# Performance work log

Hardware: AMD Instinct MI355X
Metric: run time of the kernel (lower is better)

Reference implementation:

```python
import jax, jax.numpy as jnp
import numpy as np
import math

D_MODEL = 1024
D_STATE = 16
D_CONV = 4
EXPAND = 2
D_INNER = EXPAND * D_MODEL
DT_RANK = 64
BATCH = 4
SEQ_LEN = 2048


def setup_inputs() -> dict:
    key = jax.random.key(0)
    ks = jax.random.split(key, 10)
    hidden_states = jax.random.normal(ks[0], (BATCH, SEQ_LEN, D_MODEL), jnp.float32)
    in_proj_w = jax.random.normal(ks[1], (D_MODEL, 2 * D_INNER), jnp.float32) * (D_MODEL ** -0.5)
    conv_w = jax.random.normal(ks[2], (D_INNER, D_CONV), jnp.float32) * (D_CONV ** -0.5)
    conv_b = jnp.zeros((D_INNER,), jnp.float32)
    x_proj_w = jax.random.normal(ks[3], (D_INNER, DT_RANK + 2 * D_STATE), jnp.float32) * (D_INNER ** -0.5)
    dt_init_std = DT_RANK ** -0.5
    dt_proj_w = jax.random.uniform(ks[4], (DT_RANK, D_INNER), jnp.float32, -dt_init_std, dt_init_std)
    # inverse-softplus init of dt bias: dt ~ logUniform(dt_min, dt_max)
    dt_min, dt_max, dt_floor = 0.001, 0.1, 1e-4
    dt = jnp.exp(jax.random.uniform(ks[5], (D_INNER,), jnp.float32) * (math.log(dt_max) - math.log(dt_min)) + math.log(dt_min))
    dt = jnp.clip(dt, dt_floor, None)
    dt_proj_b = dt + jnp.log(-jnp.expm1(-dt))
    A = jnp.tile(jnp.arange(1, D_STATE + 1, dtype=jnp.float32)[None, :], (D_INNER, 1))
    A_log = jnp.log(A)
    D = jnp.ones((D_INNER,), jnp.float32)
    out_proj_w = jax.random.normal(ks[6], (D_INNER, D_MODEL), jnp.float32) * (D_INNER ** -0.5)
    return {
        "hidden_states": hidden_states,
        "in_proj_w": in_proj_w,
        "conv_w": conv_w,
        "conv_b": conv_b,
        "x_proj_w": x_proj_w,
        "dt_proj_w": dt_proj_w,
        "dt_proj_b": dt_proj_b,
        "A_log": A_log,
        "D": D,
        "out_proj_w": out_proj_w,
    }


def _mamba_forward(hidden_states, in_proj_w, conv_w, conv_b, x_proj_w, dt_proj_w, dt_proj_b, A_log, D, out_proj_w):
    b, L, _ = hidden_states.shape
    d_state = A_log.shape[1]
    dt_rank = dt_proj_w.shape[0]
    K = conv_w.shape[1]

    xz = hidden_states @ in_proj_w                     # (b, L, 2*d_inner)
    x, z = jnp.split(xz, 2, axis=-1)                   # each (b, L, d_inner)

    # causal depthwise conv1d (padding = K-1, truncated to L)
    x_pad = jnp.pad(x, ((0, 0), (K - 1, 0), (0, 0)))
    x = sum(x_pad[:, k:k + L, :] * conv_w[:, k] for k in range(K)) + conv_b
    x = jax.nn.silu(x)

    x_dbl = x @ x_proj_w                               # (b, L, dt_rank + 2*d_state)
    dt, B, C = jnp.split(x_dbl, [dt_rank, dt_rank + d_state], axis=-1)
    dt = jax.nn.softplus(dt @ dt_proj_w + dt_proj_b)   # (b, L, d_inner)
    A = -jnp.exp(A_log)                                # (d_inner, d_state)

    def step(h, inp):
        x_t, dt_t, B_t, C_t = inp                      # (b,d), (b,d), (b,n), (b,n)
        dA = jnp.exp(A[None] * dt_t[..., None])        # (b, d, n)
        h = dA * h + dt_t[..., None] * B_t[:, None, :] * x_t[..., None]
        y_t = jnp.einsum('bdn,bn->bd', h, C_t) + D * x_t
        return h, y_t

    h0 = jnp.zeros((b, x.shape[-1], d_state), x.dtype)
    xs = (x.transpose(1, 0, 2), dt.transpose(1, 0, 2), B.transpose(1, 0, 2), C.transpose(1, 0, 2))
    _, ys = jax.lax.scan(step, h0, xs)                 # ys: (L, b, d_inner)
    y = ys.transpose(1, 0, 2) * jax.nn.silu(z)
    return y @ out_proj_w                              # (b, L, d_model)


def reference(hidden_states, in_proj_w, conv_w, conv_b, x_proj_w, dt_proj_w, dt_proj_b, A_log, D, out_proj_w):
    return _mamba_forward(hidden_states, in_proj_w, conv_w, conv_b, x_proj_w, dt_proj_w, dt_proj_b, A_log, D, out_proj_w)
```

## Files before the change

### kernel.cpp

```cpp
#include <hip/hip_runtime.h>
#include <hip/hip_bf16.h>


#define DM 1024
#define DS 16
#define DC 4
#define DI 2048
#define DR 64
#define NB 4
#define SL 2048
#define NTOK (NB*SL)
#define XDBL_W (DR + 2*DS)
#define CONV_R 8

typedef __hip_bfloat16 bf16;
typedef unsigned short u16;
typedef __attribute__((ext_vector_type(8))) short s8v;
typedef __attribute__((ext_vector_type(4))) float f4v;
typedef __attribute__((ext_vector_type(4))) unsigned short us4;

__device__ __forceinline__ float b2f(bf16 v) { return __bfloat162float(v); }
__device__ __forceinline__ bf16  f2b(float v) { return __float2bfloat16(v); }
__device__ __forceinline__ u16 f2u(float x) {
    union { bf16 h; u16 s; } u; u.h = f2b(x); return u.s;
}
__device__ __forceinline__ float u2f(u16 s) {
    union { bf16 h; u16 s; } u; u.s = s; return b2f(u.h);
}

__device__ __forceinline__ bool sniff_bf16(const void* Dones) {
    return ((const u16*)Dones)[0] == 0x3F80u;
}

__device__ __forceinline__ float softplus_fast(float v) {
    return fmaxf(v, 0.f) + __logf(1.f + __expf(-fabsf(v)));
}

template<int MODE>
__device__ __forceinline__ float ld(const void* p, size_t i, bool bf) {
    if (MODE == 0) return b2f(((const bf16*)p)[i]);
    if (MODE == 1) return ((const float*)p)[i];
    return bf ? b2f(((const bf16*)p)[i]) : ((const float*)p)[i];
}
template<int MODE>
__device__ __forceinline__ void st(void* p, size_t i, bool bf, float v) {
    if (MODE == 0)      { ((bf16*)p)[i] = f2b(v); }
    else if (MODE == 1) { ((float*)p)[i] = v; }
    else { if (bf) ((bf16*)p)[i] = f2b(v); else ((float*)p)[i] = v; }
}

template<int CM>
__device__ __forceinline__ void cstore(void* C, void* C2, size_t m, int n,
                                       int ldc, bool bf, float v) {
    if (CM == 3) {
        if (n < DR) ((bf16*)C2)[m * DR + n] = f2b(v);
        else        ((float*)C)[m * (2 * DS) + (n - DR)] = v;
    } else {
        st<CM>(C, m * (size_t)ldc + n, bf, v);
    }
}

#define AS1 __attribute__((address_space(1)))
#define AS3 __attribute__((address_space(3)))
__device__ __forceinline__ void gload_lds16(const void* g, void* l) {
    __builtin_amdgcn_global_load_lds((const AS1 unsigned int*)g,
                                     (AS3 unsigned int*)l, 16, 0, 0);
}

__global__ __launch_bounds__(256) void cast_bf16_kernel(
    const void* __restrict__ src, bf16* __restrict__ dst,
    const void* __restrict__ sniff)
{
    const bool bf = sniff_bf16(sniff);
    const size_t i = ((size_t)blockIdx.x * 256 + threadIdx.x) * 4;
    if (bf) {
        *(us4*)((u16*)dst + i) = *(const us4*)((const u16*)src + i);
    } else {
        const f4v f = *(const f4v*)((const float*)src + i);
        us4 o; o.x = f2u(f.x); o.y = f2u(f.y); o.z = f2u(f.z); o.w = f2u(f.w);
        *(us4*)((u16*)dst + i) = o;
    }
}

__global__ __launch_bounds__(256) void transpose_w(
    const void* __restrict__ w, bf16* __restrict__ wt,
    int K, int N, const void* __restrict__ sniff)
{
    const bool bf = sniff_bf16(sniff);
    __shared__ float t[32][33];
    const int tx = threadIdx.x & 31, ty = threadIdx.x >> 5;
    const int n0 = blockIdx.x * 32, k0 = blockIdx.y * 32;
    #pragma unroll
    for (int i = 0; i < 4; i++) {
        int k = k0 + ty + i * 8, n = n0 + tx;
        t[ty + i * 8][tx] = (n < N) ? ld<2>(w, (size_t)k * N + n, bf) : 0.f;
    }
    __syncthreads();
    #pragma unroll
    for (int i = 0; i < 4; i++) {
        int n = n0 + ty + i * 8, k = k0 + tx;
        wt[(size_t)n * K + k] = f2b(t[tx][ty + i * 8]);
    }
}

template<int CM, int EPI>
__global__ __launch_bounds__(256) void gemm_mfma(
    const bf16* __restrict__ A, int lda,
    const bf16* __restrict__ Bt,
    void* __restrict__ C, void* __restrict__ C2, int ldc,
    int M, int N, int K,
    const void* __restrict__ bias,
    const void* __restrict__ sniff)
{
    const bool bf = sniff_bf16(sniff);
    __shared__ short As[128 * 32];
    __shared__ short Bs[128 * 32];

    const int tid  = threadIdx.x;
    const int lane = tid & 63;
    const int wave = tid >> 6;
    const int wm = (wave & 1) * 64;
    const int wn = (wave >> 1) * 64;
    const int m0 = blockIdx.x * 128;
    const int n0 = blockIdx.y * 128;
    const int ll = lane & 15;
    const int qd = lane >> 4;

    const int srow  = lane >> 2;
    const int skoff = (lane & 3) * 8;

    const short* Ag = (const short*)A;
    const short* Bg = (const short*)Bt;
    char* AsB = (char*)As + wave * 2048 + lane * 16;
    char* BsB = (char*)Bs + wave * 2048 + lane * 16;
    const size_t a_row = (size_t)(m0 + wave * 32 + srow);
    const size_t b_row = (size_t)(n0 + wave * 32 + srow);

    f4v acc[4][4];
    #pragma unroll
    for (int i = 0; i < 4; i++)
        #pragma unroll
        for (int j = 0; j < 4; j++)
            acc[i][j] = (f4v){0.f, 0.f, 0.f, 0.f};

    for (int k0 = 0; k0 < K; k0 += 32) {
        gload_lds16(Ag + a_row * lda + k0 + skoff,            AsB);
        gload_lds16(Ag + (a_row + 16) * lda + k0 + skoff,     AsB + 1024);
        gload_lds16(Bg + b_row * K + k0 + skoff,              BsB);
        gload_lds16(Bg + (b_row + 16) * K + k0 + skoff,       BsB + 1024);
        __syncthreads();

        s8v af[4], bfr[4];
        #pragma unroll
        for (int s = 0; s < 4; s++)
            af[s] = *(const s8v*)&As[(wm + s * 16 + ll) * 32 + qd * 8];
        #pragma unroll
        for (int s = 0; s < 4; s++)
            bfr[s] = *(const s8v*)&Bs[(wn + s * 16 + ll) * 32 + qd * 8];
        #pragma unroll
        for (int i = 0; i < 4; i++)
            #pragma unroll
            for (int j = 0; j < 4; j++)
                acc[i][j] = __builtin_amdgcn_mfma_f32_16x16x32_bf16(
                    af[i], bfr[j], acc[i][j], 0, 0, 0);
        __syncthreads();
    }

    #pragma unroll
    for (int sn = 0; sn < 4; sn++) {
        const int cn = n0 + wn + sn * 16 + ll;
        if (cn >= N) continue;
        float bv = 0.f;
        if (EPI == 1) bv = ld<2>(bias, cn, bf);
        #pragma unroll
        for (int sm = 0; sm < 4; sm++) {
            #pragma unroll
            for (int r = 0; r < 4; r++) {
                const int cm = m0 + wm + sm * 16 + qd * 4 + r;
                float v = acc[sm][sn][r];
                if (EPI == 1) v = softplus_fast(v + bv);
                cstore<CM>(C, C2, (size_t)cm, cn, ldc, bf, v);
            }
        }
    }
}

template<int AM, int CM, int EPI>
__global__ __launch_bounds__(256) void gemm_kernel(
    const void* __restrict__ A, int lda,
    const void* __restrict__ B, size_t bbase, int ldb,
    void* __restrict__ C, void* __restrict__ C2, int ldc,
    int M, int N, int K,
    const void* __restrict__ bias,
    const void* __restrict__ sniff)
{
    const bool bf = sniff_bf16(sniff);
    const int BM = 64, BN = 64, BK = 16;
    __shared__ float Asm[BK][BM + 4];
    __shared__ float Bsm[BK][BN + 4];

    const int tid = threadIdx.x;
    const int m0 = blockIdx.x * BM;
    const int n0 = blockIdx.y * BN;
    const int tx = tid % 16;
    const int ty = tid / 16;
    const int a_k = tid % BK;
    const int a_m = tid / BK;
    const int b_n = tid % BN;
    const int b_k = tid / BN;

    float acc[4][4] = {};

    for (int k0 = 0; k0 < K; k0 += BK) {
        #pragma unroll
        for (int i = 0; i < 4; i++) {
            int m = m0 + a_m + i * 16;
            float v = 0.f;
            if (m < M) v = ld<AM>(A, (size_t)m * lda + (k0 + a_k), bf);
            Asm[a_k][a_m + i * 16] = v;
        }
        #pragma unroll
        for (int i = 0; i < 4; i++) {
            int kk = b_k + i * 4;
            int n = n0 + b_n;
            float v = 0.f;
            if (n < N) v = ld<2>(B, bbase + (size_t)(k0 + kk) * ldb + n, bf);
            Bsm[kk][b_n] = v;
        }
        __syncthreads();
        #pragma unroll
        for (int kk = 0; kk < BK; kk++) {
            float av[4], bv[4];
            #pragma unroll
            for (int i = 0; i < 4; i++) av[i] = Asm[kk][ty * 4 + i];
            #pragma unroll
            for (int j = 0; j < 4; j++) bv[j] = Bsm[kk][tx * 4 + j];
            #pragma unroll
            for (int i = 0; i < 4; i++)
                #pragma unroll
                for (int j = 0; j < 4; j++)
                    acc[i][j] += av[i] * bv[j];
        }
        __syncthreads();
    }
    #pragma unroll
    for (int i = 0; i < 4; i++) {
        int m = m0 + ty * 4 + i;
        if (m >= M) continue;
        #pragma unroll
        for (int j = 0; j < 4; j++) {
            int n = n0 + tx * 4 + j;
            if (n >= N) continue;
            float v = acc[i][j];
            if (EPI == 1) {
                v += ld<2>(bias, n, bf);
                v = softplus_fast(v);
            }
            cstore<CM>(C, C2, (size_t)m, n, ldc, bf, v);
        }
    }
}

__global__ __launch_bounds__(256) void conv_silu_kernel(
    const bf16* __restrict__ xg, const void* __restrict__ w,
    const void* __restrict__ bias, bf16* __restrict__ xc,
    const void* __restrict__ sniff)
{
    const bool bf = sniff_bf16(sniff);
    const int c  = blockIdx.x * 256 + threadIdx.x;
    const int r0 = blockIdx.y * CONV_R;
    const int l0 = r0 % SL;

    float w0, w1, w2, w3;
    if (bf) {
        const us4 wv = *(const us4*)((const u16*)w + (size_t)c * 4);
        w0 = u2f(wv.x); w1 = u2f(wv.y); w2 = u2f(wv.z); w3 = u2f(wv.w);
    } else {
        const f4v wv = *(const f4v*)((const float*)w + (size_t)c * 4);
        w0 = wv.x; w1 = wv.y; w2 = wv.z; w3 = wv.w;
    }
    const float bs = ld<2>(bias, c, bf);

    float xm3 = (l0 >= 3) ? b2f(xg[(size_t)(r0 - 3) * DI + c]) : 0.f;
    float xm2 = (l0 >= 2) ? b2f(xg[(size_t)(r0 - 2) * DI + c]) : 0.f;
    float xm1 = (l0 >= 1) ? b2f(xg[(size_t)(r0 - 1) * DI + c]) : 0.f;

    #pragma unroll
    for (int i = 0; i < CONV_R; i++) {
        const size_t row = (size_t)(r0 + i);
        const float x0 = b2f(xg[row * DI + c]);
        const float acc = bs + w0 * xm3 + w1 * xm2 + w2 * xm1 + w3 * x0;
        const float s = acc / (1.f + __expf(-acc));
        xc[row * DI + c] = f2b(s);
        xm3 = xm2; xm2 = xm1; xm1 = x0;
    }
}

__global__ __launch_bounds__(256) void scan_pass1(
    const bf16* __restrict__ xc, const bf16* __restrict__ dt,
    const float* __restrict__ bc,
    const void* __restrict__ A_log, const void* __restrict__ Dones,
    float* __restrict__ P, float* __restrict__ Q, int nch)
{
    const bool bf = sniff_bf16(Dones);
    const int d = blockIdx.x * 256 + threadIdx.x;
    const int c = blockIdx.y;
    const int b = blockIdx.z;
    const int T = SL / nch;

    float a[DS], Pp[DS], Qq[DS];
    bool lad = true;
    #pragma unroll
    for (int n = 0; n < DS; n++) {
        a[n] = -__expf(ld<2>(A_log, (size_t)d * DS + n, bf));
        Pp[n] = 1.f; Qq[n] = 0.f;
        lad = lad && (fabsf(a[n] - (n + 1) * a[0]) < 1e-3f);
    }

    const size_t base = (size_t)b * SL + (size_t)c * T;
    if (lad) {
        const float a0 = a[0];
        for (int i = 0; i < T; i++) {
            const size_t row = base + i;
            const float xv  = b2f(xc[row * DI + d]);
            const float dtv = b2f(dt[row * DI + d]);
            const float dtx = dtv * xv;
            const float* Bv = bc + row * (2 * DS);
            const float r = __expf(a0 * dtv);
            float cur = r;
            #pragma unroll
            for (int n = 0; n < DS; n++) {
                Pp[n] *= cur;
                Qq[n] = cur * Qq[n] + dtx * Bv[n];
                cur *= r;
            }
        }
    } else {
        for (int i = 0; i < T; i++) {
            const size_t row = base + i;
            const float xv  = b2f(xc[row * DI + d]);
            const float dtv = b2f(dt[row * DI + d]);
            const float dtx = dtv * xv;
            const float* Bv = bc + row * (2 * DS);
            #pragma unroll
            for (int n = 0; n < DS; n++) {
                const float dA = __expf(a[n] * dtv);
                Pp[n] *= dA;
                Qq[n] = dA * Qq[n] + dtx * Bv[n];
            }
        }
    }
    const size_t o = (((size_t)b * nch + c) * DI + d) * DS;
    #pragma unroll
    for (int n = 0; n < DS; n++) { P[o + n] = Pp[n]; Q[o + n] = Qq[n]; }
}

__global__ __launch_bounds__(256) void scan_pass2(
    float* __restrict__ P, const float* __restrict__ Q, int nch)
{
    const int j = blockIdx.x * 256 + threadIdx.x;
    const int b = blockIdx.y;
    float h = 0.f;
    for (int c = 0; c < nch; c++) {
        const size_t o = ((size_t)b * nch + c) * (DI * DS) + j;
        const float p = P[o];
        const float q = Q[o];
        P[o] = h;
        h = p * h + q;
    }
}

__global__ __launch_bounds__(256) void scan_pass3(
    const bf16* __restrict__ xc, const bf16* __restrict__ dt,
    const float* __restrict__ bc, bf16* __restrict__ z,
    const void* __restrict__ A_log, const void* __restrict__ Dones,
    const float* __restrict__ H, int nch)
{
    const bool bf = sniff_bf16(Dones);
    const int d = blockIdx.x * 256 + threadIdx.x;
    const int c = blockIdx.y;
    const int b = blockIdx.z;
    const int T = SL / nch;

    float a[DS], h[DS];
    bool lad = true;
    const size_t o = (((size_t)b * nch + c) * DI + d) * DS;
    #pragma unroll
    for (int n = 0; n < DS; n++) {
        a[n] = -__expf(ld<2>(A_log, (size_t)d * DS + n, bf));
        h[n] = H[o + n];
        lad = lad && (fabsf(a[n] - (n + 1) * a[0]) < 1e-3f);
    }
    const float dD = ld<2>(Dones, d, bf);
    const size_t base = (size_t)b * SL + (size_t)c * T;

    if (lad) {
        const float a0 = a[0];
        for (int i = 0; i < T; i++) {
            const size_t row = base + i;
            const float xv  = b2f(xc[row * DI + d]);
            const float dtv = b2f(dt[row * DI + d]);
            const float zv  = b2f(z[row * DI + d]);
            const float dtx = dtv * xv;
            const float* Bv = bc + row * (2 * DS);
            const float* Cv = Bv + DS;
            const float r = __expf(a0 * dtv);
            float cur = r;
            float y = dD * xv;
            #pragma unroll
            for (int n = 0; n < DS; n++) {
                h[n] = cur * h[n] + dtx * Bv[n];
                y += h[n] * Cv[n];
                cur *= r;
            }
            const float g = zv / (1.f + __expf(-zv));
            z[row * DI + d] = f2b(y * g);
        }
    } else {
        for (int i = 0; i < T; i++) {
            const size_t row = base + i;
            const float xv  = b2f(xc[row * DI + d]);
            const float dtv = b2f(dt[row * DI + d]);
            const float zv  = b2f(z[row * DI + d]);
            const float dtx = dtv * xv;
            const float* Bv = bc + row * (2 * DS);
            const float* Cv = Bv + DS;
            float y = dD * xv;
            #pragma unroll
            for (int n = 0; n < DS; n++) {
                const float dA = __expf(a[n] * dtv);
                h[n] = dA * h[n] + dtx * Bv[n];
                y += h[n] * Cv[n];
            }
            const float g = zv / (1.f + __expf(-zv));
            z[row * DI + d] = f2b(y * g);
        }
    }
}

__global__ __launch_bounds__(256) void scan_serial(
    const bf16* __restrict__ xc, const bf16* __restrict__ dt,
    const float* __restrict__ bc, bf16* __restrict__ z,
    const void* __restrict__ A_log, const void* __restrict__ Dones)
{
    const bool bf = sniff_bf16(Dones);
    const int d = blockIdx.x * 256 + threadIdx.x;
    const int b = blockIdx.y;
    float a[DS], h[DS];
    #pragma unroll
    for (int n = 0; n < DS; n++) {
        a[n] = -__expf(ld<2>(A_log, (size_t)d * DS + n, bf));
        h[n] = 0.f;
    }
    const float dD = ld<2>(Dones, d, bf);
    const size_t base = (size_t)b * SL;
    for (int l = 0; l < SL; l++) {
        const size_t row = base + l;
        const float xv  = b2f(xc[row * DI + d]);
        const float dtv = b2f(dt[row * DI + d]);
        const float* Bv = bc + row * (2 * DS);
        const float dtx = dtv * xv;
        float y = dD * xv;
        #pragma unroll
        for (int n = 0; n < DS; n++) {
            const float dA = __expf(a[n] * dtv);
            h[n] = dA * h[n] + dtx * Bv[n];
            y += h[n] * Bv[DS + n];
        }
        const float zv = b2f(z[row * DI + d]);
        const float g = zv / (1.f + __expf(-zv));
        z[row * DI + d] = f2b(y * g);
    }
}

extern "C" void kernel_launch(void* const* d_in, const int* in_sizes, int n_in,
                              void* d_out, int out_size, void* d_ws, size_t ws_size,
                              hipStream_t stream) {
    const void* hs        = d_in[0];
    const void* in_proj_w = d_in[1];
    const void* conv_w    = d_in[2];
    const void* conv_b    = d_in[3];
    const void* x_proj_w  = d_in[4];
    const void* dt_proj_w = d_in[5];
    const void* dt_proj_b = d_in[6];
    const void* A_log     = d_in[7];
    const void* Dones     = d_in[8];
    const void* out_proj_w= d_in[9];

    char* ws = (char*)d_ws;
    bf16*  xg   = (bf16*)(ws);
    bf16*  xc   = (bf16*)(ws + 33554432);
    bf16*  hsb  = (bf16*)(ws + 33554432);
    bf16*  z    = (bf16*)(ws + 67108864);
    float* bc   = (float*)(ws + 100663296);
    bf16*  dtf  = (bf16*)(ws + 101711872);
    const size_t WT_OFF = 102760448;
    bf16* in_projT  = (bf16*)(ws + WT_OFF);
    bf16* x_projT   = (bf16*)(ws + WT_OFF);
    bf16* dt_projT  = (bf16*)(ws + WT_OFF + 524288);
    bf16* out_projT = (bf16*)(ws + WT_OFF);
    const bool mfma_ok = ws_size >= WT_OFF + 8388608;

    const size_t per_chunk = (size_t)NB * DI * DS * 4 * 2;
    int nch = 32;
    while (nch > 1 && WT_OFF + (size_t)nch * per_chunk > ws_size) nch >>= 1;
    const bool chunked = (WT_OFF + (size_t)nch * per_chunk <= ws_size);
    float* P = (float*)(ws + WT_OFF);
    float* Q = P + (size_t)NB * nch * DI * DS;

    bf16* dtb = xg;

    if (mfma_ok) {
        cast_bf16_kernel<<<(NTOK*DM/4)/256, 256, 0, stream>>>(hs, hsb, Dones);
        transpose_w<<<dim3((2*DI)/32, DM/32), 256, 0, stream>>>(
            in_proj_w, in_projT, DM, 2*DI, Dones);
        gemm_mfma<0, 0><<<dim3(NTOK/128, DI/128), 256, 0, stream>>>(
            hsb, DM, in_projT, xg, nullptr, DI, NTOK, DI, DM, nullptr, Dones);
        gemm_mfma<0, 0><<<dim3(NTOK/128, DI/128), 256, 0, stream>>>(
            hsb, DM, in_projT + (size_t)DI * DM, z, nullptr, DI, NTOK, DI, DM,
            nullptr, Dones);
        conv_silu_kernel<<<dim3(DI/256, NTOK/CONV_R), 256, 0, stream>>>(
            xg, conv_w, conv_b, xc, Dones);
        transpose_w<<<dim3(128/32, DI/32), 256, 0, stream>>>(
            x_proj_w, x_projT, DI, XDBL_W, Dones);
        gemm_mfma<3, 0><<<dim3(NTOK/128, 1), 256, 0, stream>>>(
            xc, DI, x_projT, bc, dtf, 0, NTOK, XDBL_W, DI, nullptr, Dones);
        transpose_w<<<dim3(DI/32, DR/32), 256, 0, stream>>>(
            dt_proj_w, dt_projT, DR, DI, Dones);
        gemm_mfma<0, 1><<<dim3(NTOK/128, DI/128), 256, 0, stream>>>(
            dtf, DR, dt_projT, dtb, nullptr, DI, NTOK, DI, DR, dt_proj_b, Dones);
    } else {
        gemm_kernel<2, 0, 0><<<dim3(NTOK/64, DI/64), 256, 0, stream>>>(
            hs, DM, in_proj_w, 0, 2*DI, xg, nullptr, DI, NTOK, DI, DM, nullptr, Dones);
        gemm_kernel<2, 0, 0><<<dim3(NTOK/64, DI/64), 256, 0, stream>>>(
            hs, DM, in_proj_w, DI, 2*DI, z, nullptr, DI, NTOK, DI, DM, nullptr, Dones);
        conv_silu_kernel<<<dim3(DI/256, NTOK/CONV_R), 256, 0, stream>>>(
            xg, conv_w, conv_b, xc, Dones);
        gemm_kernel<0, 3, 0><<<dim3(NTOK/64, (XDBL_W + 63)/64), 256, 0, stream>>>(
            xc, DI, x_proj_w, 0, XDBL_W, bc, dtf, 0, NTOK, XDBL_W, DI, nullptr, Dones);
        gemm_kernel<0, 0, 1><<<dim3(NTOK/64, DI/64), 256, 0, stream>>>(
            dtf, DR, dt_proj_w, 0, DI, dtb, nullptr, DI, NTOK, DI, DR, dt_proj_b, Dones);
    }

    if (chunked) {
        scan_pass1<<<dim3(DI/256, nch, NB), 256, 0, stream>>>(
            xc, dtb, bc, A_log, Dones, P, Q, nch);
        scan_pass2<<<dim3((DI*DS)/256, NB), 256, 0, stream>>>(P, Q, nch);
        scan_pass3<<<dim3(DI/256, nch, NB), 256, 0, stream>>>(
            xc, dtb, bc, z, A_log, Dones, P, nch);
    } else {
        scan_serial<<<dim3(DI/256, NB), 256, 0, stream>>>(
            xc, dtb, bc, z, A_log, Dones);
    }

    if (mfma_ok) {
        transpose_w<<<dim3(DM/32, DI/32), 256, 0, stream>>>(
            out_proj_w, out_projT, DI, DM, Dones);
        gemm_mfma<2, 0><<<dim3(NTOK/128, DM/128), 256, 0, stream>>>(
            z, DI, out_projT, d_out, nullptr, DM, NTOK, DM, DI, nullptr, Dones);
    } else {
        gemm_kernel<0, 2, 0><<<dim3(NTOK/64, DM/64), 256, 0, stream>>>(
            z, DI, out_proj_w, 0, DM, d_out, nullptr, DM, NTOK, DM, DI, nullptr, Dones);
    }
}
```

Measured before the change: 506.3 us.

## Add double-buffered large-tile MFMA GEMM with direct global-to-LDS loads

Adds a new GEMM kernel with 256x256 or 256x128 block tiles, 512 threads, K-step 64, and double-buffered LDS. Next-tile loads go straight from global memory to LDS and are issued while the current tile's MFMAs run, with an XOR swizzle to avoid bank conflicts and setprio around the MFMA bursts. The in_proj and out_proj GEMMs now use it to get more reuse per block and hide load latency. In exchange it uses much more LDS per block, has fewer blocks (occupancy and tail effects), and assumes the dimensions divide the tile sizes.

```diff
diff --git a/kernel.cpp b/kernel.cpp
--- a/kernel.cpp
+++ b/kernel.cpp
@@ -103,6 +103,124 @@
     }
 }
 
+template<int BM, int BN, int WM, int WN, int CM>
+__global__ __launch_bounds__(WM*WN*64, 2) void gemm_big(
+    const bf16* __restrict__ A, int lda,
+    const bf16* __restrict__ Bt,
+    void* __restrict__ C, int ldc, int K,
+    const void* __restrict__ sniff)
+{
+    constexpr int NT  = WM * WN;
+    constexpr int NTH = NT * 64;
+    constexpr int WAVE_M = BM / WM, WAVE_N = BN / WN;
+    constexpr int MR = WAVE_M / 16, NR = WAVE_N / 16, MR2 = MR / 2;
+    constexpr int CH_ROWS = NTH / 8;
+    constexpr int ACH = BM / CH_ROWS;
+    constexpr int BCH = BN / CH_ROWS;
+
+    const bool bf = sniff_bf16(sniff);
+    __shared__ short Asm[2][BM * 64];
+    __shared__ short Bsm[2][BN * 64];
+
+    const int tid = threadIdx.x, lane = tid & 63, wave = tid >> 6;
+    const int wm = wave / WN, wn = wave % WN;
+    const int ll = lane & 15, qd = lane >> 4;
+    const int m0 = blockIdx.x * BM, n0 = blockIdx.y * BN;
+
+    const int s_r  = tid >> 3;
+    const int s_cb = ((tid & 7) * 16) ^ ((s_r & 7) << 4);
+
+    const char* Ab = (const char*)A;
+    const char* Bb = (const char*)Bt;
+
+    f4v acc[MR][NR];
+    #pragma unroll
+    for (int i = 0; i < MR; i++)
+        #pragma unroll
+        for (int j = 0; j < NR; j++) acc[i][j] = (f4v){0.f, 0.f, 0.f, 0.f};
+
+    #pragma unroll
+    for (int c = 0; c < ACH; c++)
+        gload_lds16(Ab + (((size_t)(m0 + c * CH_ROWS + s_r) * lda) << 1) + s_cb,
+                    (char*)&Asm[0][0] + (c * NTH + tid) * 16);
+    #pragma unroll
+    for (int c = 0; c < BCH; c++)
+        gload_lds16(Bb + (((size_t)(n0 + c * CH_ROWS + s_r) * K) << 1) + s_cb,
+                    (char*)&Bsm[0][0] + (c * NTH + tid) * 16);
+    asm volatile("s_waitcnt vmcnt(0)" ::: "memory");
+    __builtin_amdgcn_sched_barrier(0);
+    __builtin_amdgcn_s_barrier();
+
+    const int NTILE = K >> 6;
+    for (int t = 0; t < NTILE; ++t) {
+        const int cur = t & 1, nxt = cur ^ 1;
+        const int kk = (t + 1) << 6;
+        const bool more = (t + 1 < NTILE);
+        const char* Ac = (const char*)&Asm[cur][0];
+        const char* Bc = (const char*)&Bsm[cur][0];
+        #pragma unroll
+        for (int p = 0; p < 4; ++p) {
+            const int kh = p >> 1, mh = p & 1;
+            const int kb = kh * 64;
+            s8v af[MR2], bv[NR];
+            #pragma unroll
+            for (int i = 0; i < MR2; i++) {
+                const int row = wm * WAVE_M + (mh * MR2 + i) * 16 + ll;
+                af[i] = *(const s8v*)(Ac + (size_t)row * 128
+                                        + ((kb + qd * 16) ^ ((ll & 7) << 4)));
+            }
+            #pragma unroll
+            for (int j = 0; j < NR; j++) {
+                const int row = wn * WAVE_N + j * 16 + ll;
+                bv[j] = *(const s8v*)(Bc + (size_t)row * 128
+                                        + ((kb + qd * 16) ^ ((ll & 7) << 4)));
+            }
+            if (p == 0 && more) {
+                #pragma unroll
+                for (int c = 0; c < ACH; c++)
+                    gload_lds16(Ab + (((size_t)(m0 + c * CH_ROWS + s_r) * lda + kk) << 1) + s_cb,
+                                (char*)&Asm[nxt][0] + (c * NTH + tid) * 16);
+            }
+            if (p == 1 && more) {
+                #pragma unroll
+                for (int c = 0; c < BCH; c++)
+                    gload_lds16(Bb + (((size_t)(n0 + c * CH_ROWS + s_r) * K + kk) << 1) + s_cb,
+                                (char*)&Bsm[nxt][0] + (c * NTH + tid) * 16);
+            }
+            __builtin_amdgcn_sched_barrier(0);
+            __builtin_amdgcn_s_barrier();
+            asm volatile("s_waitcnt lgkmcnt(0)" ::: "memory");
+            __builtin_amdgcn_sched_barrier(0);
+            __builtin_amdgcn_s_setprio(1);
+            #pragma unroll
+            for (int i = 0; i < MR2; i++)
+                #pragma unroll
+                for (int j = 0; j < NR; j++)
+                    acc[mh * MR2 + i][j] = __builtin_amdgcn_mfma_f32_16x16x32_bf16(
+                        af[i], bv[j], acc[mh * MR2 + i][j], 0, 0, 0);
+            __builtin_amdgcn_s_setprio(0);
+            if (p == 3) {
+                asm volatile("s_waitcnt vmcnt(0)" ::: "memory");
+            }
+            __builtin_amdgcn_sched_barrier(0);
+            __builtin_amdgcn_s_barrier();
+        }
+    }
+
+    #pragma unroll
+    for (int i = 0; i < MR; i++) {
+        #pragma unroll
+        for (int j = 0; j < NR; j++) {
+            const int col = n0 + wn * WAVE_N + j * 16 + ll;
+            #pragma unroll
+            for (int r = 0; r < 4; r++) {
+                const int row = m0 + wm * WAVE_M + i * 16 + qd * 4 + r;
+                st<CM>(C, (size_t)row * ldc + col, bf, acc[i][j][r]);
+            }
+        }
+    }
+}
+
 template<int CM, int EPI>
 __global__ __launch_bounds__(256) void gemm_mfma(
     const bf16* __restrict__ A, int lda,
@@ -170,15 +288,15 @@
     for (int sn = 0; sn < 4; sn++) {
         const int cn = n0 + wn + sn * 16 + ll;
         if (cn >= N) continue;
-        float bv = 0.f;
-        if (EPI == 1) bv = ld<2>(bias, cn, bf);
+        float bvv = 0.f;
+        if (EPI == 1) bvv = ld<2>(bias, cn, bf);
         #pragma unroll
         for (int sm = 0; sm < 4; sm++) {
             #pragma unroll
             for (int r = 0; r < 4; r++) {
                 const int cm = m0 + wm + sm * 16 + qd * 4 + r;
                 float v = acc[sm][sn][r];
-                if (EPI == 1) v = softplus_fast(v + bv);
+                if (EPI == 1) v = softplus_fast(v + bvv);
                 cstore<CM>(C, C2, (size_t)cm, cn, ldc, bf, v);
             }
         }
@@ -514,11 +632,10 @@
         cast_bf16_kernel<<<(NTOK*DM/4)/256, 256, 0, stream>>>(hs, hsb, Dones);
         transpose_w<<<dim3((2*DI)/32, DM/32), 256, 0, stream>>>(
             in_proj_w, in_projT, DM, 2*DI, Dones);
-        gemm_mfma<0, 0><<<dim3(NTOK/128, DI/128), 256, 0, stream>>>(
-            hsb, DM, in_projT, xg, nullptr, DI, NTOK, DI, DM, nullptr, Dones);
-        gemm_mfma<0, 0><<<dim3(NTOK/128, DI/128), 256, 0, stream>>>(
-            hsb, DM, in_projT + (size_t)DI * DM, z, nullptr, DI, NTOK, DI, DM,
-            nullptr, Dones);
+        gemm_big<256, 256, 2, 4, 0><<<dim3(NTOK/256, DI/256), 512, 0, stream>>>(
+            hsb, DM, in_projT, xg, DI, DM, Dones);
+        gemm_big<256, 256, 2, 4, 0><<<dim3(NTOK/256, DI/256), 512, 0, stream>>>(
+            hsb, DM, in_projT + (size_t)DI * DM, z, DI, DM, Dones);
         conv_silu_kernel<<<dim3(DI/256, NTOK/CONV_R), 256, 0, stream>>>(
             xg, conv_w, conv_b, xc, Dones);
         transpose_w<<<dim3(128/32, DI/32), 256, 0, stream>>>(
@@ -556,8 +673,8 @@
     if (mfma_ok) {
         transpose_w<<<dim3(DM/32, DI/32), 256, 0, stream>>>(
             out_proj_w, out_projT, DI, DM, Dones);
-        gemm_mfma<2, 0><<<dim3(NTOK/128, DM/128), 256, 0, stream>>>(
-            z, DI, out_projT, d_out, nullptr, DM, NTOK, DM, DI, nullptr, Dones);
+        gemm_big<256, 128, 4, 2, 2><<<dim3(NTOK/256, DM/128), 512, 0, stream>>>(
+            z, DI, out_projT, d_out, DM, DI, Dones);
     } else {
         gemm_kernel<0, 2, 0><<<dim3(NTOK/64, DM/64), 256, 0, stream>>>(
             z, DI, out_proj_w, 0, DM, d_out, nullptr, DM, NTOK, DM, DI, nullptr, Dones);
```

Measured after the change: 464.3 us. 1.09x faster.
